# Kernel optimization log

Hardware: AMD Instinct MI355X
Metric: run time of the kernel (lower is better)

## Reference

```python
import jax, jax.numpy as jnp
import numpy as np

D_MODEL = 1024
H = 16
D_FF = 2048
EPS = 1e-5


def _ln(x, g, b):
    m = jnp.mean(x, axis=-1, keepdims=True)
    v = jnp.mean((x - m) ** 2, axis=-1, keepdims=True)
    return (x - m) * jax.lax.rsqrt(v + EPS) * g + b


def setup_inputs() -> dict:
    key = jax.random.key(0)
    ks = jax.random.split(key, 16)
    d, dff = D_MODEL, D_FF
    s = 1.0 / np.sqrt(d)
    inp = {
        "x": jax.random.normal(ks[0], (2, 2048, d), jnp.float32),
        "Wq": jax.random.normal(ks[1], (d, d), jnp.float32) * s,
        "bq": jax.random.normal(ks[2], (d,), jnp.float32) * 0.01,
        "Wk": jax.random.normal(ks[3], (d, d), jnp.float32) * s,
        "bk": jax.random.normal(ks[4], (d,), jnp.float32) * 0.01,
        "Wv": jax.random.normal(ks[5], (d, d), jnp.float32) * s,
        "bv": jax.random.normal(ks[6], (d,), jnp.float32) * 0.01,
        "Wo": jax.random.normal(ks[7], (d, d), jnp.float32) * s,
        "bo": jax.random.normal(ks[8], (d,), jnp.float32) * 0.01,
        "ln1_g": 1.0 + 0.1 * jax.random.normal(ks[9], (d,), jnp.float32),
        "ln1_b": 0.01 * jax.random.normal(ks[10], (d,), jnp.float32),
        "ln2_g": 1.0 + 0.1 * jax.random.normal(ks[11], (d,), jnp.float32),
        "ln2_b": 0.01 * jax.random.normal(ks[12], (d,), jnp.float32),
        "W1": jax.random.normal(ks[13], (d, dff), jnp.float32) * s,
        "b1": 0.01 * jax.random.normal(ks[14], (dff,), jnp.float32),
        "W2": jax.random.normal(ks[15], (dff, d), jnp.float32) * (1.0 / np.sqrt(dff)),
        "b2": jnp.zeros((d,), jnp.float32),
    }
    return inp


def reference(x, Wq, bq, Wk, bk, Wv, bv, Wo, bo, ln1_g, ln1_b, ln2_g, ln2_b, W1, b1, W2, b2):
    b, s, d = x.shape
    dk = d // H

    # --- sublayer 1: pre-LN self-attention with residual (dropout = eval/identity) ---
    y = _ln(x, ln1_g, ln1_b)
    q = (y @ Wq + bq).reshape(b, s, H, dk).transpose(0, 2, 1, 3)  # (b,h,s,dk)
    k = (y @ Wk + bk).reshape(b, s, H, dk).transpose(0, 2, 1, 3)
    v = (y @ Wv + bv).reshape(b, s, H, dk).transpose(0, 2, 1, 3)
    scores = jnp.einsum("bhqd,bhkd->bhqk", q, k) / jnp.sqrt(jnp.float32(dk))
    attn = jax.nn.softmax(scores, axis=-1)
    o = jnp.einsum("bhqk,bhkd->bhqd", attn, v)  # (b,h,s,dk)
    # faithful to original bug: transpose last two dims then flat reshape
    o = jnp.swapaxes(o, -1, -2).reshape(b, s, d)  # (b,h,dk,s) -> (b,s,d)
    x = x + (o @ Wo + bo)

    # --- sublayer 2: pre-LN FFN with residual ---
    y2 = _ln(x, ln2_g, ln2_b)
    f = jax.nn.relu(y2 @ W1 + b1) @ W2 + b2
    return x + f
```

## Files before the change

### kernel.cpp

```cpp
#include <hip/hip_runtime.h>
#include <hip/hip_bf16.h>

#define D_MODEL 1024
#define NHEAD 16
#define DK 64
#define DFF 2048
#define SEQ 2048
#define NBATCH 2
#define NTOK (NBATCH*SEQ)

typedef __attribute__((ext_vector_type(8))) short bf16x8;
typedef __attribute__((ext_vector_type(4))) float f32x4;
typedef __attribute__((ext_vector_type(16))) float f32x16;
typedef __attribute__((ext_vector_type(4))) short s16x4;

#if __has_builtin(__builtin_amdgcn_exp2f)
#define EXP2(x) __builtin_amdgcn_exp2f(x)
#else
#define EXP2(x) exp2f(x)
#endif

__device__ __forceinline__ short f2bf(float f) {
    union { float f; unsigned u; } v; v.f = f;
    unsigned r = v.u + 0x7FFFu + ((v.u >> 16) & 1u);
    return (short)(r >> 16);
}

__device__ __forceinline__ void gld16(void* lds, const void* g) {
    __builtin_amdgcn_global_load_lds(
        (const __attribute__((address_space(1))) void*)g,
        (__attribute__((address_space(3))) void*)lds, 16, 0, 0);
}

__global__ __launch_bounds__(256) void k_transpose(const float* __restrict__ W,
                                                   short* __restrict__ WT, int K, int N)
{
    __shared__ float t[32][33];
    int tid = threadIdx.x;
    int n0 = blockIdx.x * 32, k0 = blockIdx.y * 32;
#pragma unroll
    for (int p = 0; p < 4; ++p) {
        int idx = p * 256 + tid, r = idx >> 5, c = idx & 31;
        t[r][c] = W[(size_t)(k0 + r) * N + (n0 + c)];
    }
    __syncthreads();
#pragma unroll
    for (int p = 0; p < 4; ++p) {
        int idx = p * 256 + tid, r = idx >> 5, c = idx & 31;
        WT[(size_t)(n0 + r) * K + (k0 + c)] = f2bf(t[c][r]);
    }
}

struct TP4 { const float* src[4]; short* dst[4]; };
__global__ __launch_bounds__(256) void k_transpose4(TP4 tp)
{
    __shared__ float t[32][33];
    const float* W = tp.src[blockIdx.z];
    short* WT = tp.dst[blockIdx.z];
    const int K = 1024, N = 1024;
    int tid = threadIdx.x;
    int n0 = blockIdx.x * 32, k0 = blockIdx.y * 32;
#pragma unroll
    for (int p = 0; p < 4; ++p) {
        int idx = p * 256 + tid, r = idx >> 5, c = idx & 31;
        t[r][c] = W[(size_t)(k0 + r) * N + (n0 + c)];
    }
    __syncthreads();
#pragma unroll
    for (int p = 0; p < 4; ++p) {
        int idx = p * 256 + tid, r = idx >> 5, c = idx & 31;
        WT[(size_t)(n0 + r) * K + (k0 + c)] = f2bf(t[c][r]);
    }
}

__global__ __launch_bounds__(256) void k_layernorm(const float* __restrict__ x,
                                                   const float* __restrict__ g,
                                                   const float* __restrict__ bta,
                                                   short* __restrict__ y)
{
    int row = blockIdx.x * 4 + (threadIdx.x >> 6);
    int lane = threadIdx.x & 63;
    const float* xr = x + (size_t)row * D_MODEL;
    float4 v[4];
    float s = 0.f, s2 = 0.f;
#pragma unroll
    for (int c = 0; c < 4; ++c) {
        v[c] = *(const float4*)(xr + c * 256 + lane * 4);
        s  += v[c].x + v[c].y + v[c].z + v[c].w;
        s2 += v[c].x * v[c].x + v[c].y * v[c].y + v[c].z * v[c].z + v[c].w * v[c].w;
    }
#pragma unroll
    for (int off = 1; off < 64; off <<= 1) {
        s  += __shfl_xor(s, off, 64);
        s2 += __shfl_xor(s2, off, 64);
    }
    float mean = s * (1.f / 1024.f);
    float var  = s2 * (1.f / 1024.f) - mean * mean;
    float rs = rsqrtf(var + 1e-5f);
    short* yr = y + (size_t)row * D_MODEL;
#pragma unroll
    for (int c = 0; c < 4; ++c) {
        int idx = c * 256 + lane * 4;
        float4 gg = *(const float4*)(g + idx);
        float4 bb = *(const float4*)(bta + idx);
        s16x4 o;
        o.x = f2bf((v[c].x - mean) * rs * gg.x + bb.x);
        o.y = f2bf((v[c].y - mean) * rs * gg.y + bb.y);
        o.z = f2bf((v[c].z - mean) * rs * gg.z + bb.z);
        o.w = f2bf((v[c].w - mean) * rs * gg.w + bb.w);
        *(s16x4*)(yr + idx) = o;
    }
}

template<int EPI, int BN, int THREADS>
__global__ __launch_bounds__(THREADS, (THREADS == 512) ? 6 : 4) void k_gemm(
    const short* __restrict__ A, const short* __restrict__ BT, int N, int K,
    const float* __restrict__ bias, const float* __restrict__ bias2, const float* __restrict__ bias3,
    const float* __restrict__ resid, float* __restrict__ outF,
    short* __restrict__ outB, short* __restrict__ outQ, short* __restrict__ outK, short* __restrict__ outV)
{
    constexpr int CW = (THREADS == 512) ? 4 : 2;
    __shared__ __align__(16) short sA[3][128 * 32];
    __shared__ __align__(16) short sB[3][BN * 32];
    int tid = threadIdx.x;
    int lane = tid & 63, wid = tid >> 6;
    int wr = wid / CW, wc = wid % CW;
    int lrow = lane & 15;
    int lk16 = (lane >> 4) << 4;

    int gx = gridDim.x;
    int nwg = gx * gridDim.y;
    int orig = blockIdx.x + blockIdx.y * gx;
    int wg = (orig & 7) * (nwg >> 3) + (orig >> 3);
    int bx = wg % gx, by = wg / gx;

    const short* Ab = A + (size_t)by * 128 * K;
    const short* Bb = BT + (size_t)bx * BN * K;

    auto src = [&](const short* base, int cc) {
        int r = cc >> 2, s = cc & 3;
        return (const char*)(base + (size_t)r * K) + ((s ^ ((r >> 1) & 3)) << 4);
    };
    const char *pA0 = src(Ab, tid), *pA1 = nullptr, *pB0;
    if constexpr (THREADS == 512) {
        pB0 = src(Bb, tid);
    } else {
        pA1 = src(Ab, 256 + tid);
        pB0 = src(Bb, tid & (BN * 4 - 1));
    }

    auto stage = [&](int buf) {
        if constexpr (THREADS == 512) {
            gld16(&sA[buf][tid * 8], pA0);  pA0 += 64;
            gld16(&sB[buf][tid * 8], pB0);  pB0 += 64;
        } else {
            gld16(&sA[buf][tid * 8], pA0);          pA0 += 64;
            gld16(&sA[buf][(256 + tid) * 8], pA1);  pA1 += 64;
            gld16(&sB[buf][(tid & (BN * 4 - 1)) * 8], pB0);  pB0 += 64;
        }
    };

    const f32x4 fz = {0.f, 0.f, 0.f, 0.f};
    f32x4 acc[4][2];
#pragma unroll
    for (int i = 0; i < 4; i++)
#pragma unroll
        for (int j = 0; j < 2; j++) acc[i][j] = fz;

    const int NT = K / 32;
    stage(0);
    stage(1);
    int cur = 0;
    for (int t = 0; t < NT; ++t) {
        if (t + 1 < NT) {
            if constexpr (THREADS == 512) asm volatile("s_waitcnt vmcnt(2)" ::: "memory");
            else                          asm volatile("s_waitcnt vmcnt(3)" ::: "memory");
        } else {
            asm volatile("s_waitcnt vmcnt(0)" ::: "memory");
        }
        __builtin_amdgcn_s_barrier();
        if (t + 2 < NT) {
            int nb3 = cur + 2; if (nb3 >= 3) nb3 -= 3;
            stage(nb3);
        }
        bf16x8 bfr[2];
#pragma unroll
        for (int j = 0; j < 2; j++) {
            int row = wc * 32 + j * 16 + lrow;
            bfr[j] = *(const bf16x8*)((const char*)sB[cur] + row * 64 + (lk16 ^ (((row >> 1) & 3) << 4)));
        }
#pragma unroll
        for (int i = 0; i < 4; i++) {
            int row = wr * 64 + i * 16 + lrow;
            bf16x8 af = *(const bf16x8*)((const char*)sA[cur] + row * 64 + (lk16 ^ (((row >> 1) & 3) << 4)));
            acc[i][0] = __builtin_amdgcn_mfma_f32_16x16x32_bf16(af, bfr[0], acc[i][0], 0, 0, 0);
            acc[i][1] = __builtin_amdgcn_mfma_f32_16x16x32_bf16(af, bfr[1], acc[i][1], 0, 0, 0);
        }
        ++cur; if (cur >= 3) cur = 0;
    }

    int m_base = by * 128 + wr * 64 + (lane >> 4) * 4;
    int n_base = bx * BN + wc * 32 + lrow;
#pragma unroll
    for (int i = 0; i < 4; i++) {
#pragma unroll
        for (int j = 0; j < 2; j++) {
            int n = n_base + j * 16;
#pragma unroll
            for (int jj = 0; jj < 4; jj++) {
                int m = m_base + i * 16 + jj;
                float v = acc[i][j][jj];
                if constexpr (EPI == 0) {
                    int seg = n >> 10, nn = n & 1023;
                    int b = m >> 11, ss = m & 2047;
                    int h = nn >> 6, dd = nn & 63;
                    if (seg == 0) {
                        outQ[(((size_t)(b * NHEAD + h)) * SEQ + ss) * DK + dd] =
                            f2bf((v + bias[nn]) * 0.18033688011112042f);
                    } else if (seg == 1) {
                        outK[(((size_t)(b * NHEAD + h)) * SEQ + ss) * DK + dd] = f2bf(v + bias2[nn]);
                    } else {
                        outV[(((size_t)(b * NHEAD + h)) * DK + dd) * SEQ + ss] = f2bf(v + bias3[nn]);
                    }
                } else if constexpr (EPI == 1) {
                    size_t idx = (size_t)m * N + n;
                    outF[idx] = v + bias[n] + resid[idx];
                } else if constexpr (EPI == 2) {
                    float r2 = v + bias[n];
                    outB[(size_t)m * N + n] = f2bf(r2 > 0.f ? r2 : 0.f);
                } else {
                    size_t idx = (size_t)m * N + n;
                    outF[idx] = v + bias[n] + resid[idx];
                }
            }
        }
    }
}

__global__ __launch_bounds__(256) void k_attn(const short* __restrict__ Q, const short* __restrict__ Kk,
                                              const short* __restrict__ Vt, short* __restrict__ Operm)
{
    __shared__ __align__(16) short sMem[2][2][64 * 64];
    int tid = threadIdx.x, lane = tid & 63;
    int wid = tid >> 6;
    int qg = wid >> 1, ks = wid & 1;
    int l31 = lane & 31, hi = lane >> 5;

    int orig = blockIdx.x + blockIdx.y * 32;
    int lg = (orig & 7) * 128 + (orig >> 3);
    int bh = lg >> 5, qt = lg & 31;
    int b = bh >> 4, h = bh & 15;
    int q0 = qt * 64 + qg * 32;
    const short* Qp = Q + (size_t)bh * SEQ * DK;
    const short* Kp = Kk + (size_t)bh * SEQ * DK;
    const short* Vp = Vt + (size_t)bh * DK * SEQ;

    bf16x8 qf[4];
#pragma unroll
    for (int kb = 0; kb < 4; ++kb)
        qf[kb] = *(const bf16x8*)(Qp + (size_t)(q0 + l31) * DK + kb * 16 + hi * 8);

    int c0 = tid, c1 = 256 + tid;
    int r0 = c0 >> 3, r1 = c1 >> 3;
    const char* pK0 = (const char*)(Kp + (size_t)r0 * DK) + (((c0 & 7) ^ (r0 & 7)) << 4);
    const char* pK1 = (const char*)(Kp + (size_t)r1 * DK) + (((c1 & 7) ^ (r1 & 7)) << 4);
    const char* pV0 = (const char*)(Vp + (size_t)r0 * SEQ) + (((c0 & 7) ^ (r0 & 7)) << 4);
    const char* pV1 = (const char*)(Vp + (size_t)r1 * SEQ) + (((c1 & 7) ^ (r1 & 7)) << 4);

    auto stage = [&](int buf) {
        gld16(&sMem[buf][0][c0 * 8], pK0);  pK0 += 8192;
        gld16(&sMem[buf][0][c1 * 8], pK1);  pK1 += 8192;
        gld16(&sMem[buf][1][c0 * 8], pV0);  pV0 += 128;
        gld16(&sMem[buf][1][c1 * 8], pV1);  pV1 += 128;
    };

    f32x16 Oa0 = {0,0,0,0,0,0,0,0,0,0,0,0,0,0,0,0};
    f32x16 Oa1 = {0,0,0,0,0,0,0,0,0,0,0,0,0,0,0,0};
    float lsum = 0.f;

    const int NT = SEQ / 64;
    int krow = ks * 32 + l31;
    int sw = (l31 & 7) << 4;

    auto pv_step = [&](unsigned a0, unsigned a1, unsigned b0v, unsigned b1v, int kslice,
                       const char* sVc) {
        asm("v_permlane32_swap_b32 %0, %1" : "+v"(a0), "+v"(b0v));
        asm("v_permlane32_swap_b32 %0, %1" : "+v"(a1), "+v"(b1v));
        union { unsigned u[4]; bf16x8 v; } pa;
        pa.u[0] = a0; pa.u[1] = a1; pa.u[2] = b0v; pa.u[3] = b1v;
        int cb = (kslice * 32 + hi * 16) ^ sw;
        bf16x8 vf0 = *(const bf16x8*)(sVc + l31 * 128 + cb);
        bf16x8 vf1 = *(const bf16x8*)(sVc + (32 + l31) * 128 + cb);
        Oa0 = __builtin_amdgcn_mfma_f32_32x32x16_bf16(pa.v, vf0, Oa0, 0, 0, 0);
        Oa1 = __builtin_amdgcn_mfma_f32_32x32x16_bf16(pa.v, vf1, Oa1, 0, 0, 0);
    };

    auto tile = [&](int t, int cur) {
        if (t + 1 < NT) {
            stage(cur ^ 1);
            asm volatile("s_waitcnt vmcnt(4)" ::: "memory");
        } else {
            asm volatile("s_waitcnt vmcnt(0)" ::: "memory");
        }
        __builtin_amdgcn_s_barrier();
        const char* sKc = (const char*)sMem[cur][0];
        const char* sVc = (const char*)sMem[cur][1];

        f32x16 sc = {0,0,0,0,0,0,0,0,0,0,0,0,0,0,0,0};
        __builtin_amdgcn_s_setprio(1);
#pragma unroll
        for (int kb = 0; kb < 4; ++kb) {
            int cb = (kb * 32 + hi * 16) ^ sw;
            bf16x8 kf = *(const bf16x8*)(sKc + krow * 128 + cb);
            sc = __builtin_amdgcn_mfma_f32_32x32x16_bf16(kf, qf[kb], sc, 0, 0, 0);
        }
        __builtin_amdgcn_s_setprio(0);

        unsigned W[4][2];
#pragma unroll
        for (int tt = 0; tt < 4; ++tt) {
            float pa_ = EXP2(sc[4*tt+0]), pb_ = EXP2(sc[4*tt+1]);
            float pc_ = EXP2(sc[4*tt+2]), pd_ = EXP2(sc[4*tt+3]);
            lsum += (pa_ + pb_) + (pc_ + pd_);
            asm("v_cvt_pk_bf16_f32 %0, %1, %2" : "=v"(W[tt][0]) : "v"(pa_), "v"(pb_));
            asm("v_cvt_pk_bf16_f32 %0, %1, %2" : "=v"(W[tt][1]) : "v"(pc_), "v"(pd_));
        }

        __builtin_amdgcn_s_setprio(1);
        pv_step(W[0][0], W[0][1], W[1][0], W[1][1], ks * 2 + 0, sVc);
        pv_step(W[2][0], W[2][1], W[3][0], W[3][1], ks * 2 + 1, sVc);
        __builtin_amdgcn_s_setprio(0);
        __builtin_amdgcn_s_barrier();
    };

    stage(0);
    for (int t = 0; t < NT; t += 2) {
        tile(t, 0);
        tile(t + 1, 1);
    }

    lsum += __shfl_xor(lsum, 32, 64);

    float* mrg = (float*)sMem;
    if (ks == 1) {
        float* m0 = mrg + (qg * 64 + lane) * 33;
#pragma unroll
        for (int i = 0; i < 16; ++i) m0[i] = Oa0[i];
#pragma unroll
        for (int i = 0; i < 16; ++i) m0[16 + i] = Oa1[i];
        m0[32] = lsum;
    }
    __syncthreads();
    if (ks == 0) {
        const float* m0 = mrg + (qg * 64 + lane) * 33;
#pragma unroll
        for (int i = 0; i < 16; ++i) Oa0[i] += m0[i];
#pragma unroll
        for (int i = 0; i < 16; ++i) Oa1[i] += m0[16 + i];
        lsum += m0[32];

        float rlv[16];
#pragma unroll
        for (int tt = 0; tt < 4; ++tt)
#pragma unroll
            for (int rr = 0; rr < 4; ++rr) {
                float ts = __shfl(lsum, 4 * hi + 8 * tt + rr, 64);
                rlv[4 * tt + rr] = 1.f / ts;
            }

        int qcol = (q0 & 1023) + 4 * hi;
        int qhi = q0 >> 10;
#pragma unroll
        for (int db = 0; db < 2; ++db) {
            const f32x16& O = db ? Oa1 : Oa0;
            int dd = db * 32 + l31;
            size_t rowoff = ((size_t)b * SEQ + h * 128 + 2 * dd + qhi) * D_MODEL + qcol;
#pragma unroll
            for (int tt = 0; tt < 4; ++tt) {
                s16x4 o;
                o.x = f2bf(O[4*tt+0] * rlv[4*tt+0]);
                o.y = f2bf(O[4*tt+1] * rlv[4*tt+1]);
                o.z = f2bf(O[4*tt+2] * rlv[4*tt+2]);
                o.w = f2bf(O[4*tt+3] * rlv[4*tt+3]);
                *(s16x4*)(Operm + rowoff + 8 * tt) = o;
            }
        }
    }
}

extern "C" void kernel_launch(void* const* d_in, const int* in_sizes, int n_in,
                              void* d_out, int out_size, void* d_ws, size_t ws_size,
                              hipStream_t stream)
{
    const float* x   = (const float*)d_in[0];
    const float* Wq  = (const float*)d_in[1];
    const float* bq  = (const float*)d_in[2];
    const float* Wk  = (const float*)d_in[3];
    const float* bk  = (const float*)d_in[4];
    const float* Wv  = (const float*)d_in[5];
    const float* bv  = (const float*)d_in[6];
    const float* Wo  = (const float*)d_in[7];
    const float* bo  = (const float*)d_in[8];
    const float* g1  = (const float*)d_in[9];
    const float* b1l = (const float*)d_in[10];
    const float* g2  = (const float*)d_in[11];
    const float* b2l = (const float*)d_in[12];
    const float* W1  = (const float*)d_in[13];
    const float* b1  = (const float*)d_in[14];
    const float* W2  = (const float*)d_in[15];
    const float* b2  = (const float*)d_in[16];
    float* out = (float*)d_out;

    char* ws = (char*)d_ws;
    size_t off = 0;
    auto alloc = [&](size_t bytes) {
        char* p = ws + off;
        off += (bytes + 255) & ~(size_t)255;
        return p;
    };
    short* WqkvT = (short*)alloc((size_t)3072 * 1024 * 2);
    short* WoT   = (short*)alloc((size_t)1024 * 1024 * 2);
    short* W1T   = (short*)alloc((size_t)2048 * 1024 * 2);
    short* W2T   = (short*)alloc((size_t)1024 * 2048 * 2);
    short* Y     = (short*)alloc((size_t)NTOK * 1024 * 2);
    short* Qb    = (short*)alloc((size_t)NTOK * 1024 * 2);
    short* Kb    = (short*)alloc((size_t)NTOK * 1024 * 2);
    short* Vtb   = (short*)alloc((size_t)NTOK * 1024 * 2);
    short* Operm = (short*)alloc((size_t)NTOK * 1024 * 2);
    float* X1    = (float*)alloc((size_t)NTOK * 1024 * 4);
    short* F1    = (short*)alloc((size_t)NTOK * 2048 * 2);

    TP4 tp;
    tp.src[0] = Wq; tp.dst[0] = WqkvT;
    tp.src[1] = Wk; tp.dst[1] = WqkvT + 1024 * 1024;
    tp.src[2] = Wv; tp.dst[2] = WqkvT + 2048 * 1024;
    tp.src[3] = Wo; tp.dst[3] = WoT;
    k_transpose4<<<dim3(32, 32, 4), 256, 0, stream>>>(tp);
    k_transpose<<<dim3(64, 32), 256, 0, stream>>>(W1, W1T, 1024, 2048);
    k_transpose<<<dim3(32, 64), 256, 0, stream>>>(W2, W2T, 2048, 1024);

    k_layernorm<<<NTOK / 4, 256, 0, stream>>>(x, g1, b1l, Y);

    k_gemm<0,128,512><<<dim3(24, 32), 512, 0, stream>>>(Y, WqkvT, 3072, 1024,
        bq, bk, bv, nullptr, nullptr, nullptr, Qb, Kb, Vtb);

    k_attn<<<dim3(32, 32), 256, 0, stream>>>(Qb, Kb, Vtb, Operm);

    k_gemm<1,64,256><<<dim3(16, 32), 256, 0, stream>>>(Operm, WoT, 1024, 1024,
        bo, nullptr, nullptr, x, X1, nullptr, nullptr, nullptr, nullptr);

    k_layernorm<<<NTOK / 4, 256, 0, stream>>>(X1, g2, b2l, Y);

    k_gemm<2,128,512><<<dim3(16, 32), 512, 0, stream>>>(Y, W1T, 2048, 1024,
        b1, nullptr, nullptr, nullptr, nullptr, F1, nullptr, nullptr, nullptr);

    k_gemm<3,64,256><<<dim3(16, 32), 256, 0, stream>>>(F1, W2T, 1024, 2048,
        b2, nullptr, nullptr, X1, out, nullptr, nullptr, nullptr, nullptr);
}
```

Baseline: 201.5 us.

## Merge weight transposes into one launch and restage GEMM prefetch with extra barrier

Merges the three weight-transpose launches into a single 8192-block kernel that works out its segment from a flat block index, removing launch overhead. In the GEMM main loop, the next-next tile is now issued before the wait-and-barrier, and a second barrier after the MFMAs guards against overwriting a buffer still being read. The 512-thread GEMM's occupancy hint rises from 6 to 8 waves. The attention loop is rewritten from a two-tile unrolled lambda into a plain loop with the PV step as an inner lambda, which may change code generation. The extra barrier per K step adds sync cost, and the higher occupancy hint may force register spills.

```diff
diff --git a/kernel.cpp b/kernel.cpp
--- a/kernel.cpp
+++ b/kernel.cpp
@@ -32,34 +32,21 @@
         (__attribute__((address_space(3))) void*)lds, 16, 0, 0);
 }
 
-__global__ __launch_bounds__(256) void k_transpose(const float* __restrict__ W,
-                                                   short* __restrict__ WT, int K, int N)
+struct TP6 { const float* src[6]; short* dst[6]; int K[6], N[6], nx[6]; };
+__global__ __launch_bounds__(256) void k_transpose6(TP6 tp)
 {
     __shared__ float t[32][33];
+    int id = blockIdx.x;
+    int seg, tt;
+    if (id < 4096)      { seg = id >> 10; tt = id & 1023; }
+    else if (id < 6144) { seg = 4; tt = id - 4096; }
+    else                { seg = 5; tt = id - 6144; }
+    const float* W = tp.src[seg];
+    short* WT = tp.dst[seg];
+    int K = tp.K[seg], N = tp.N[seg], nx = tp.nx[seg];
+    int bx = tt % nx, by = tt / nx;
     int tid = threadIdx.x;
-    int n0 = blockIdx.x * 32, k0 = blockIdx.y * 32;
-#pragma unroll
-    for (int p = 0; p < 4; ++p) {
-        int idx = p * 256 + tid, r = idx >> 5, c = idx & 31;
-        t[r][c] = W[(size_t)(k0 + r) * N + (n0 + c)];
-    }
-    __syncthreads();
-#pragma unroll
-    for (int p = 0; p < 4; ++p) {
-        int idx = p * 256 + tid, r = idx >> 5, c = idx & 31;
-        WT[(size_t)(n0 + r) * K + (k0 + c)] = f2bf(t[c][r]);
-    }
-}
-
-struct TP4 { const float* src[4]; short* dst[4]; };
-__global__ __launch_bounds__(256) void k_transpose4(TP4 tp)
-{
-    __shared__ float t[32][33];
-    const float* W = tp.src[blockIdx.z];
-    short* WT = tp.dst[blockIdx.z];
-    const int K = 1024, N = 1024;
-    int tid = threadIdx.x;
-    int n0 = blockIdx.x * 32, k0 = blockIdx.y * 32;
+    int n0 = bx * 32, k0 = by * 32;
 #pragma unroll
     for (int p = 0; p < 4; ++p) {
         int idx = p * 256 + tid, r = idx >> 5, c = idx & 31;
@@ -113,7 +100,7 @@
 }
 
 template<int EPI, int BN, int THREADS>
-__global__ __launch_bounds__(THREADS, (THREADS == 512) ? 6 : 4) void k_gemm(
+__global__ __launch_bounds__(THREADS, (THREADS == 512) ? 8 : 4) void k_gemm(
     const short* __restrict__ A, const short* __restrict__ BT, int N, int K,
     const float* __restrict__ bias, const float* __restrict__ bias2, const float* __restrict__ bias3,
     const float* __restrict__ resid, float* __restrict__ outF,
@@ -172,17 +159,18 @@
     stage(1);
     int cur = 0;
     for (int t = 0; t < NT; ++t) {
-        if (t + 1 < NT) {
+        if (t + 2 < NT) {
+            int nb3 = cur + 2; if (nb3 >= 3) nb3 -= 3;
+            stage(nb3);
+            if constexpr (THREADS == 512) asm volatile("s_waitcnt vmcnt(4)" ::: "memory");
+            else                          asm volatile("s_waitcnt vmcnt(6)" ::: "memory");
+        } else if (t + 1 < NT) {
             if constexpr (THREADS == 512) asm volatile("s_waitcnt vmcnt(2)" ::: "memory");
             else                          asm volatile("s_waitcnt vmcnt(3)" ::: "memory");
         } else {
             asm volatile("s_waitcnt vmcnt(0)" ::: "memory");
         }
         __builtin_amdgcn_s_barrier();
-        if (t + 2 < NT) {
-            int nb3 = cur + 2; if (nb3 >= 3) nb3 -= 3;
-            stage(nb3);
-        }
         bf16x8 bfr[2];
 #pragma unroll
         for (int j = 0; j < 2; j++) {
@@ -196,6 +184,7 @@
             acc[i][0] = __builtin_amdgcn_mfma_f32_16x16x32_bf16(af, bfr[0], acc[i][0], 0, 0, 0);
             acc[i][1] = __builtin_amdgcn_mfma_f32_16x16x32_bf16(af, bfr[1], acc[i][1], 0, 0, 0);
         }
+        __builtin_amdgcn_s_barrier();
         ++cur; if (cur >= 3) cur = 0;
     }
 
@@ -278,24 +267,12 @@
     f32x16 Oa1 = {0,0,0,0,0,0,0,0,0,0,0,0,0,0,0,0};
     float lsum = 0.f;
 
+    stage(0);
     const int NT = SEQ / 64;
     int krow = ks * 32 + l31;
     int sw = (l31 & 7) << 4;
-
-    auto pv_step = [&](unsigned a0, unsigned a1, unsigned b0v, unsigned b1v, int kslice,
-                       const char* sVc) {
-        asm("v_permlane32_swap_b32 %0, %1" : "+v"(a0), "+v"(b0v));
-        asm("v_permlane32_swap_b32 %0, %1" : "+v"(a1), "+v"(b1v));
-        union { unsigned u[4]; bf16x8 v; } pa;
-        pa.u[0] = a0; pa.u[1] = a1; pa.u[2] = b0v; pa.u[3] = b1v;
-        int cb = (kslice * 32 + hi * 16) ^ sw;
-        bf16x8 vf0 = *(const bf16x8*)(sVc + l31 * 128 + cb);
-        bf16x8 vf1 = *(const bf16x8*)(sVc + (32 + l31) * 128 + cb);
-        Oa0 = __builtin_amdgcn_mfma_f32_32x32x16_bf16(pa.v, vf0, Oa0, 0, 0, 0);
-        Oa1 = __builtin_amdgcn_mfma_f32_32x32x16_bf16(pa.v, vf1, Oa1, 0, 0, 0);
-    };
-
-    auto tile = [&](int t, int cur) {
+    for (int t = 0; t < NT; ++t) {
+        int cur = t & 1;
         if (t + 1 < NT) {
             stage(cur ^ 1);
             asm volatile("s_waitcnt vmcnt(4)" ::: "memory");
@@ -326,17 +303,22 @@
             asm("v_cvt_pk_bf16_f32 %0, %1, %2" : "=v"(W[tt][1]) : "v"(pc_), "v"(pd_));
         }
 
+        auto pv_step = [&](unsigned a0, unsigned a1, unsigned b0v, unsigned b1v, int kslice) {
+            asm("v_permlane32_swap_b32 %0, %1" : "+v"(a0), "+v"(b0v));
+            asm("v_permlane32_swap_b32 %0, %1" : "+v"(a1), "+v"(b1v));
+            union { unsigned u[4]; bf16x8 v; } pa;
+            pa.u[0] = a0; pa.u[1] = a1; pa.u[2] = b0v; pa.u[3] = b1v;
+            int cb = (kslice * 32 + hi * 16) ^ sw;
+            bf16x8 vf0 = *(const bf16x8*)(sVc + l31 * 128 + cb);
+            bf16x8 vf1 = *(const bf16x8*)(sVc + (32 + l31) * 128 + cb);
+            Oa0 = __builtin_amdgcn_mfma_f32_32x32x16_bf16(pa.v, vf0, Oa0, 0, 0, 0);
+            Oa1 = __builtin_amdgcn_mfma_f32_32x32x16_bf16(pa.v, vf1, Oa1, 0, 0, 0);
+        };
         __builtin_amdgcn_s_setprio(1);
-        pv_step(W[0][0], W[0][1], W[1][0], W[1][1], ks * 2 + 0, sVc);
-        pv_step(W[2][0], W[2][1], W[3][0], W[3][1], ks * 2 + 1, sVc);
+        pv_step(W[0][0], W[0][1], W[1][0], W[1][1], ks * 2 + 0);
+        pv_step(W[2][0], W[2][1], W[3][0], W[3][1], ks * 2 + 1);
         __builtin_amdgcn_s_setprio(0);
         __builtin_amdgcn_s_barrier();
-    };
-
-    stage(0);
-    for (int t = 0; t < NT; t += 2) {
-        tile(t, 0);
-        tile(t + 1, 1);
     }
 
     lsum += __shfl_xor(lsum, 32, 64);
@@ -430,14 +412,14 @@
     float* X1    = (float*)alloc((size_t)NTOK * 1024 * 4);
     short* F1    = (short*)alloc((size_t)NTOK * 2048 * 2);
 
-    TP4 tp;
-    tp.src[0] = Wq; tp.dst[0] = WqkvT;
-    tp.src[1] = Wk; tp.dst[1] = WqkvT + 1024 * 1024;
-    tp.src[2] = Wv; tp.dst[2] = WqkvT + 2048 * 1024;
-    tp.src[3] = Wo; tp.dst[3] = WoT;
-    k_transpose4<<<dim3(32, 32, 4), 256, 0, stream>>>(tp);
-    k_transpose<<<dim3(64, 32), 256, 0, stream>>>(W1, W1T, 1024, 2048);
-    k_transpose<<<dim3(32, 64), 256, 0, stream>>>(W2, W2T, 2048, 1024);
+    TP6 tp;
+    tp.src[0] = Wq; tp.dst[0] = WqkvT;                tp.K[0] = 1024; tp.N[0] = 1024; tp.nx[0] = 32;
+    tp.src[1] = Wk; tp.dst[1] = WqkvT + 1024 * 1024;  tp.K[1] = 1024; tp.N[1] = 1024; tp.nx[1] = 32;
+    tp.src[2] = Wv; tp.dst[2] = WqkvT + 2048 * 1024;  tp.K[2] = 1024; tp.N[2] = 1024; tp.nx[2] = 32;
+    tp.src[3] = Wo; tp.dst[3] = WoT;                  tp.K[3] = 1024; tp.N[3] = 1024; tp.nx[3] = 32;
+    tp.src[4] = W1; tp.dst[4] = W1T;                  tp.K[4] = 1024; tp.N[4] = 2048; tp.nx[4] = 64;
+    tp.src[5] = W2; tp.dst[5] = W2T;                  tp.K[5] = 2048; tp.N[5] = 1024; tp.nx[5] = 32;
+    k_transpose6<<<8192, 256, 0, stream>>>(tp);
 
     k_layernorm<<<NTOK / 4, 256, 0, stream>>>(x, g1, b1l, Y);
 
```

New measurement: 197.1 us. 2.2% less time.
